# Kernel tuning notes

Hardware: AMD Instinct MI355X
Metric: run time of the kernel (lower is better)

The kernel has to match this reference:

```python
import jax, jax.numpy as jnp
import numpy as np

KH, KW, STRIDE, PAD = 3, 3, 1, 1
TREE_DEPTH = 3
NUM_LEAVES = 2 ** TREE_DEPTH  # 8
NUM_NODES = NUM_LEAVES - 1    # 7
OUT_CH, IN_CH = 256, 64
B, H, W = 16, 48, 48
PATCH_LEN = IN_CH * KH * KW   # 576

# Each of the 16 relaxed binary logic gates g_k(a,b) is affine in (1, a, b, a*b):
#   g_k(a,b) = c0 + c1*a + c2*b + c3*(a*b)
# Rows follow the standard difflogic gate ordering (gate 3 = pass-through a).
GATE_COEFF = np.array([
    [0.,  0.,  0.,  0.],   # 0: FALSE
    [0.,  0.,  0.,  1.],   # 1: a AND b
    [0.,  1.,  0., -1.],   # 2: a AND NOT b
    [0.,  1.,  0.,  0.],   # 3: a
    [0.,  0.,  1., -1.],   # 4: NOT a AND b
    [0.,  0.,  1.,  0.],   # 5: b
    [0.,  1.,  1., -2.],   # 6: a XOR b
    [0.,  1.,  1., -1.],   # 7: a OR b
    [1., -1., -1.,  1.],   # 8: NOT (a OR b)
    [1., -1., -1.,  2.],   # 9: NOT (a XOR b)
    [1.,  0., -1.,  0.],   # 10: NOT b
    [1.,  0., -1.,  1.],   # 11: a OR NOT b
    [1., -1.,  0.,  0.],   # 12: NOT a
    [1., -1.,  0.,  1.],   # 13: NOT a OR b
    [1.,  0.,  0., -1.],   # 14: NOT (a AND b)
    [1.,  0.,  0.,  0.],   # 15: TRUE
], dtype=np.float32)


def _unfold(x):
    # x: (B, C, Hp, Wp) -> (B, C*KH*KW, Ho*Wo), channel-major then row-major
    # kernel ordering (matches torch.nn.functional.unfold).
    b, c, hp, wp = x.shape
    ho = (hp - KH) // STRIDE + 1
    wo = (wp - KW) // STRIDE + 1
    cols = jnp.stack(
        [x[:, :, i:i + STRIDE * ho:STRIDE, j:j + STRIDE * wo:STRIDE]
         for i in range(KH) for j in range(KW)], axis=2)  # (B, C, KH*KW, Ho, Wo)
    return cols.reshape(b, c * KH * KW, ho * wo), ho, wo


def setup_inputs() -> dict:
    key = jax.random.key(0)
    k1, k2, k3 = jax.random.split(key, 3)
    x = jax.random.uniform(k1, (B, IN_CH, H, W), dtype=jnp.float32)
    logits = jax.random.normal(k2, (OUT_CH, NUM_NODES, 16), dtype=jnp.float32)
    leaf_indices = jax.random.randint(k3, (OUT_CH, NUM_LEAVES), 0, PATCH_LEN, dtype=jnp.int32)
    return {"x": x, "logits": logits, "leaf_indices": leaf_indices}


def reference(x, logits, leaf_indices):
    b = x.shape[0]
    o = logits.shape[0]
    xp = jnp.pad(x, ((0, 0), (0, 0), (PAD, PAD), (PAD, PAD)))
    patches, ho, wo = _unfold(xp)          # (B, patch_len, L)
    cur = patches[:, leaf_indices, :]      # gather leaves: (B, O, num_leaves, L)
    coeff = jnp.asarray(GATE_COEFF)        # (16, 4)
    node_ptr = 0
    width = NUM_LEAVES
    for _ in range(TREE_DEPTH):
        nc = width // 2
        a = cur[:, :, 0::2, :]             # (B, O, nc, L)
        bb = cur[:, :, 1::2, :]
        probs = jax.nn.softmax(logits[:, node_ptr:node_ptr + nc, :], axis=-1)  # (O, nc, 16)
        # softmax-weighted mixture of the 16 gates = affine combo in (1, a, b, ab)
        w = jnp.einsum('ong,gc->onc', probs, coeff)  # (O, nc, 4)
        w = w[None, :, :, :, None]                   # (1, O, nc, 4, 1)
        cur = w[:, :, :, 0] + w[:, :, :, 1] * a + w[:, :, :, 2] * bb + w[:, :, :, 3] * (a * bb)
        node_ptr += nc
        width = nc
    y = cur[:, :, 0, :]                    # (B, O, L)
    return y.reshape(b, o, ho, wo)
```

## Files before the change

kernel.cpp:

```cpp
#include <hip/hip_runtime.h>

#define NB 16
#define IN_CH 64
#define OUT_CH 256
#define NH 48
#define NW 48
#define NPIX (NH * NW)
#define ROW_STRIDE 52
#define CH_STRIDE (4 * ROW_STRIDE)
#define LDS_DW (IN_CH * CH_STRIDE)
#define NITEMS (IN_CH * 4 * 26)
#define META_F4 9

__constant__ float c_gate[16 * 4] = {
    0.f, 0.f, 0.f, 0.f,
    0.f, 0.f, 0.f, 1.f,
    0.f, 1.f, 0.f, -1.f,
    0.f, 1.f, 0.f, 0.f,
    0.f, 0.f, 1.f, -1.f,
    0.f, 0.f, 1.f, 0.f,
    0.f, 1.f, 1.f, -2.f,
    0.f, 1.f, 1.f, -1.f,
    1.f, -1.f, -1.f, 1.f,
    1.f, -1.f, -1.f, 2.f,
    1.f, 0.f, -1.f, 0.f,
    1.f, 0.f, -1.f, 1.f,
    1.f, -1.f, 0.f, 0.f,
    1.f, -1.f, 0.f, 1.f,
    1.f, 0.f, 0.f, -1.f,
    1.f, 0.f, 0.f, 0.f
};

__global__ __launch_bounds__(256) void prep_kernel(
    const float* __restrict__ logits,
    const int*   __restrict__ leaf_idx,
    float*       __restrict__ meta)
{
    int t = blockIdx.x * 256 + threadIdx.x;
    if (t < OUT_CH * 8) {
        int idx = leaf_idx[t];
        int c  = idx / 9;
        int k  = idx - c * 9;
        int di = k / 3;
        int dj = k - di * 3;
        reinterpret_cast<int*>(meta)[(t >> 3) * 36 + (t & 7)] =
            c * CH_STRIDE + di * ROW_STRIDE + dj;
    } else {
        int t2 = t - OUT_CH * 8;
        if (t2 >= OUT_CH * 7) return;
        int o = t2 / 7;
        int n = t2 - o * 7;
        const float* lg = logits + (size_t)t2 * 16;

        float m = lg[0];
#pragma unroll
        for (int g = 1; g < 16; ++g) m = fmaxf(m, lg[g]);
        float e16[16];
        float s = 0.f;
#pragma unroll
        for (int g = 0; g < 16; ++g) { e16[g] = expf(lg[g] - m); s += e16[g]; }
        float inv = 1.f / s;

        float w0 = 0.f, w1 = 0.f, w2 = 0.f, w3 = 0.f;
#pragma unroll
        for (int g = 0; g < 16; ++g) {
            float p = e16[g] * inv;
            w0 += p * c_gate[g * 4 + 0];
            w1 += p * c_gate[g * 4 + 1];
            w2 += p * c_gate[g * 4 + 2];
            w3 += p * c_gate[g * 4 + 3];
        }
        float* mw = meta + o * 36 + 8 + n * 4;
        mw[0] = w0; mw[1] = w1; mw[2] = w2; mw[3] = w3;
    }
}

#define LTC_BODY(MC, MN)                                                        \
    {                                                                           \
        _Pragma("unroll")                                                       \
        for (int q = 0; q < 9; ++q) MN[q] = mptr[9 + q];                        \
        const int off0 = __float_as_int(MC[0].x);                               \
        const int off1 = __float_as_int(MC[0].y);                               \
        const int off2 = __float_as_int(MC[0].z);                               \
        const int off3 = __float_as_int(MC[0].w);                               \
        const int off4 = __float_as_int(MC[1].x);                               \
        const int off5 = __float_as_int(MC[1].y);                               \
        const int off6 = __float_as_int(MC[1].z);                               \
        const int off7 = __float_as_int(MC[1].w);                               \
        _Pragma("unroll")                                                       \
        for (int g = 0; g < 3; ++g) {                                           \
            const int bg = bases[g];                                            \
            float v0 = lds[off0 + bg];                                          \
            float v1 = lds[off1 + bg];                                          \
            float v2 = lds[off2 + bg];                                          \
            float v3 = lds[off3 + bg];                                          \
            float v4 = lds[off4 + bg];                                          \
            float v5 = lds[off5 + bg];                                          \
            float v6 = lds[off6 + bg];                                          \
            float v7 = lds[off7 + bg];                                          \
            float t0 = fmaf(v1, fmaf(MC[2].w, v0, MC[2].z), fmaf(MC[2].y, v0, MC[2].x)); \
            float t1 = fmaf(v3, fmaf(MC[3].w, v2, MC[3].z), fmaf(MC[3].y, v2, MC[3].x)); \
            float t2 = fmaf(v5, fmaf(MC[4].w, v4, MC[4].z), fmaf(MC[4].y, v4, MC[4].x)); \
            float t3 = fmaf(v7, fmaf(MC[5].w, v6, MC[5].z), fmaf(MC[5].y, v6, MC[5].x)); \
            float u0 = fmaf(t1, fmaf(MC[6].w, t0, MC[6].z), fmaf(MC[6].y, t0, MC[6].x)); \
            float u1 = fmaf(t3, fmaf(MC[7].w, t2, MC[7].z), fmaf(MC[7].y, t2, MC[7].x)); \
            float y  = fmaf(u1, fmaf(MC[8].w, u0, MC[8].z), fmaf(MC[8].y, u0, MC[8].x)); \
            pbase[opx[g]] = y;                                                  \
        }                                                                       \
        mptr  += 9;                                                             \
        pbase += NPIX;                                                          \
    }

__global__ __launch_bounds__(256) void ltc_kernel(
    const float*  __restrict__ x,
    const float4* __restrict__ meta,
    float*        __restrict__ out)
{
    __shared__ float lds[LDS_DW];

    const int band  = blockIdx.x;
    const int ohalf = blockIdx.y;
    const int b     = blockIdx.z;
    const int r0    = band * 2;
    const int tid   = threadIdx.x;

    const float* xb = x + (size_t)b * IN_CH * NPIX;
    for (int it = tid; it < NITEMS; it += 256) {
        int c   = it / 104;
        int rem = it - c * 104;
        int r4  = rem / 26;
        int p   = rem - r4 * 26;
        int gr  = r0 - 1 + r4;
        float2 v = make_float2(0.f, 0.f);
        if (p > 0 && p < 25 && (unsigned)gr < NH)
            v = *reinterpret_cast<const float2*>(xb + (c * NH + gr) * NW + (2 * p - 2));
        *reinterpret_cast<float2*>(&lds[c * CH_STRIDE + r4 * ROW_STRIDE + 2 * p]) = v;
    }
    __syncthreads();

    const int lane = tid & 63;
    const int wid  = tid >> 6;
    const int og   = lane >> 5;
    const int pxg  = lane & 31;
    const int o0   = ohalf * 128 + (wid * 2 + og) * 16;

    int bases[3], opx[3];
#pragma unroll
    for (int g = 0; g < 3; ++g) {
        int px = g * 32 + pxg;
        int rr = (px >= 48) ? 1 : 0;
        int cc = px - rr * 48;
        bases[g] = rr * ROW_STRIDE + cc + 1;
        opx[g]   = (r0 + rr) * NW + cc;
    }

    const float4* mptr = meta + (size_t)o0 * META_F4;
    float*        pbase = out + ((size_t)b * OUT_CH + o0) * NPIX;

    float4 A[9], Bv[9];
#pragma unroll
    for (int q = 0; q < 9; ++q) A[q] = mptr[q];

#pragma unroll 1
    for (int i = 0; i < 8; ++i) {
        LTC_BODY(A, Bv)
        LTC_BODY(Bv, A)
    }
}

extern "C" void kernel_launch(void* const* d_in, const int* in_sizes, int n_in,
                              void* d_out, int out_size, void* d_ws, size_t ws_size,
                              hipStream_t stream) {
    const float* x        = (const float*)d_in[0];
    const float* logits   = (const float*)d_in[1];
    const int*   leaf_idx = (const int*)d_in[2];
    float*       out      = (float*)d_out;
    float*       meta     = (float*)d_ws;

    prep_kernel<<<15, 256, 0, stream>>>(logits, leaf_idx, meta);

    dim3 grid(24, 2, NB);
    ltc_kernel<<<grid, 256, 0, stream>>>(x, (const float4*)meta, out);
}
```

Before: 38.44 us.

## Use 512-thread blocks with half the output channels per wave, drop meta prefetch

Doubles the block size to 512 threads so each wave handles 8 output channels instead of 16, which halves the serial per-wave loop and spreads the work over more waves sharing the same LDS tile. The manual double-buffered register prefetch of per-channel metadata is replaced by a simple per-iteration load with unroll 2, lowering register pressure to fit the new launch bounds. The risk is exposed latency on the metadata loads now that explicit prefetching is gone, and 512-thread blocks with about 53KB LDS each may limit how many blocks fit per CU.

```diff
diff --git a/kernel.cpp b/kernel.cpp
--- a/kernel.cpp
+++ b/kernel.cpp
@@ -75,43 +75,7 @@
     }
 }
 
-#define LTC_BODY(MC, MN)                                                        \
-    {                                                                           \
-        _Pragma("unroll")                                                       \
-        for (int q = 0; q < 9; ++q) MN[q] = mptr[9 + q];                        \
-        const int off0 = __float_as_int(MC[0].x);                               \
-        const int off1 = __float_as_int(MC[0].y);                               \
-        const int off2 = __float_as_int(MC[0].z);                               \
-        const int off3 = __float_as_int(MC[0].w);                               \
-        const int off4 = __float_as_int(MC[1].x);                               \
-        const int off5 = __float_as_int(MC[1].y);                               \
-        const int off6 = __float_as_int(MC[1].z);                               \
-        const int off7 = __float_as_int(MC[1].w);                               \
-        _Pragma("unroll")                                                       \
-        for (int g = 0; g < 3; ++g) {                                           \
-            const int bg = bases[g];                                            \
-            float v0 = lds[off0 + bg];                                          \
-            float v1 = lds[off1 + bg];                                          \
-            float v2 = lds[off2 + bg];                                          \
-            float v3 = lds[off3 + bg];                                          \
-            float v4 = lds[off4 + bg];                                          \
-            float v5 = lds[off5 + bg];                                          \
-            float v6 = lds[off6 + bg];                                          \
-            float v7 = lds[off7 + bg];                                          \
-            float t0 = fmaf(v1, fmaf(MC[2].w, v0, MC[2].z), fmaf(MC[2].y, v0, MC[2].x)); \
-            float t1 = fmaf(v3, fmaf(MC[3].w, v2, MC[3].z), fmaf(MC[3].y, v2, MC[3].x)); \
-            float t2 = fmaf(v5, fmaf(MC[4].w, v4, MC[4].z), fmaf(MC[4].y, v4, MC[4].x)); \
-            float t3 = fmaf(v7, fmaf(MC[5].w, v6, MC[5].z), fmaf(MC[5].y, v6, MC[5].x)); \
-            float u0 = fmaf(t1, fmaf(MC[6].w, t0, MC[6].z), fmaf(MC[6].y, t0, MC[6].x)); \
-            float u1 = fmaf(t3, fmaf(MC[7].w, t2, MC[7].z), fmaf(MC[7].y, t2, MC[7].x)); \
-            float y  = fmaf(u1, fmaf(MC[8].w, u0, MC[8].z), fmaf(MC[8].y, u0, MC[8].x)); \
-            pbase[opx[g]] = y;                                                  \
-        }                                                                       \
-        mptr  += 9;                                                             \
-        pbase += NPIX;                                                          \
-    }
-
-__global__ __launch_bounds__(256) void ltc_kernel(
+__global__ __launch_bounds__(512, 6) void ltc_kernel(
     const float*  __restrict__ x,
     const float4* __restrict__ meta,
     float*        __restrict__ out)
@@ -125,7 +89,7 @@
     const int tid   = threadIdx.x;
 
     const float* xb = x + (size_t)b * IN_CH * NPIX;
-    for (int it = tid; it < NITEMS; it += 256) {
+    for (int it = tid; it < NITEMS; it += 512) {
         int c   = it / 104;
         int rem = it - c * 104;
         int r4  = rem / 26;
@@ -142,7 +106,7 @@
     const int wid  = tid >> 6;
     const int og   = lane >> 5;
     const int pxg  = lane & 31;
-    const int o0   = ohalf * 128 + (wid * 2 + og) * 16;
+    const int o0   = ohalf * 128 + ((wid << 1) | og) * 8;
 
     int bases[3], opx[3];
 #pragma unroll
@@ -154,17 +118,46 @@
         opx[g]   = (r0 + rr) * NW + cc;
     }
 
-    const float4* mptr = meta + (size_t)o0 * META_F4;
+    const float4* mptr  = meta + (size_t)o0 * META_F4;
     float*        pbase = out + ((size_t)b * OUT_CH + o0) * NPIX;
 
-    float4 A[9], Bv[9];
+#pragma unroll 2
+    for (int i = 0; i < 8; ++i) {
+        float4 M[9];
 #pragma unroll
-    for (int q = 0; q < 9; ++q) A[q] = mptr[q];
+        for (int q = 0; q < 9; ++q) M[q] = mptr[q];
 
-#pragma unroll 1
-    for (int i = 0; i < 8; ++i) {
-        LTC_BODY(A, Bv)
-        LTC_BODY(Bv, A)
+        const int off0 = __float_as_int(M[0].x);
+        const int off1 = __float_as_int(M[0].y);
+        const int off2 = __float_as_int(M[0].z);
+        const int off3 = __float_as_int(M[0].w);
+        const int off4 = __float_as_int(M[1].x);
+        const int off5 = __float_as_int(M[1].y);
+        const int off6 = __float_as_int(M[1].z);
+        const int off7 = __float_as_int(M[1].w);
+
+#pragma unroll
+        for (int g = 0; g < 3; ++g) {
+            const int bg = bases[g];
+            float v0 = lds[off0 + bg];
+            float v1 = lds[off1 + bg];
+            float v2 = lds[off2 + bg];
+            float v3 = lds[off3 + bg];
+            float v4 = lds[off4 + bg];
+            float v5 = lds[off5 + bg];
+            float v6 = lds[off6 + bg];
+            float v7 = lds[off7 + bg];
+            float t0 = fmaf(v1, fmaf(M[2].w, v0, M[2].z), fmaf(M[2].y, v0, M[2].x));
+            float t1 = fmaf(v3, fmaf(M[3].w, v2, M[3].z), fmaf(M[3].y, v2, M[3].x));
+            float t2 = fmaf(v5, fmaf(M[4].w, v4, M[4].z), fmaf(M[4].y, v4, M[4].x));
+            float t3 = fmaf(v7, fmaf(M[5].w, v6, M[5].z), fmaf(M[5].y, v6, M[5].x));
+            float u0 = fmaf(t1, fmaf(M[6].w, t0, M[6].z), fmaf(M[6].y, t0, M[6].x));
+            float u1 = fmaf(t3, fmaf(M[7].w, t2, M[7].z), fmaf(M[7].y, t2, M[7].x));
+            float y  = fmaf(u1, fmaf(M[8].w, u0, M[8].z), fmaf(M[8].y, u0, M[8].x));
+            pbase[opx[g]] = y;
+        }
+        mptr  += META_F4;
+        pbase += NPIX;
     }
 }
 
@@ -180,5 +173,5 @@
     prep_kernel<<<15, 256, 0, stream>>>(logits, leaf_idx, meta);
 
     dim3 grid(24, 2, NB);
-    ltc_kernel<<<grid, 256, 0, stream>>>(x, (const float4*)meta, out);
+    ltc_kernel<<<grid, 512, 0, stream>>>(x, (const float4*)meta, out);
 }
```

After: 33.49 us. 12.9% less time.
